# Kernel tuning notes

Measured on AMD Instinct MI355X. Metric: run time of the kernel, lower is better.

The kernel has to match this reference:

```python
import jax, jax.numpy as jnp
import numpy as np

# conv_ada hyperparameters from init_kwargs: ka=1, alpha=0.25, kw=0.2
KA1 = 1.0          # activation scale for conv1 (ka)
KA2 = 1.25         # activation scale for conv2 (ka + alpha)
KW = 0.2           # weight clipping threshold used by the binary weight STE


def ste_sign(x, clip=1.0):
    """Binary sign with straight-through estimator (hardtanh-style clip).
    Forward value is sign(x); gradient is that of clip(x, -clip, clip)."""
    xc = jnp.clip(x, -clip, clip)
    return xc + jax.lax.stop_gradient(jnp.sign(x) - xc)


def conv_bin(x, w, ka, kw):
    """1-bit activation / 1-bit weight 3x3 conv (conv_ada).
    Activations -> ka * sign(x); weights -> per-out-channel mean(|w|) * sign(w)."""
    xq = ka * ste_sign(x)
    alpha_w = jnp.mean(jnp.abs(w), axis=(1, 2, 3), keepdims=True)  # [O,1,1,1]
    wq = alpha_w * ste_sign(w, kw)
    return jax.lax.conv_general_dilated(
        xq, wq, window_strides=(1, 1), padding='SAME',
        dimension_numbers=('NCHW', 'OIHW', 'NCHW'))


def prelu(x, slope):
    # per-channel PReLU, slope shape [C]
    return jnp.where(x >= 0, x, slope[None, :, None, None] * x)


def pixel_shuffle(x, r=2):
    b, c, h, w = x.shape
    co = c // (r * r)
    x = x.reshape(b, co, r, r, h, w)
    x = x.transpose(0, 1, 4, 2, 5, 3)  # b, co, h, r, w, r
    return x.reshape(b, co, h * r, w * r)


def setup_inputs() -> dict:
    key = jax.random.key(0)
    ks = jax.random.split(key, 11)
    B, C, H, W = 8, 64, 256, 256
    return {
        'x': jax.random.normal(ks[0], (B, C, H, W), jnp.float32),
        'w1': jax.random.normal(ks[1], (C, C, 3, 3), jnp.float32) * 0.1,
        'w2': jax.random.normal(ks[2], (2 * C, C, 3, 3), jnp.float32) * 0.1,
        'b_in': jax.random.normal(ks[3], (1, C, 1, 1), jnp.float32) * 0.01,
        'b1': jax.random.normal(ks[4], (1, C, 1, 1), jnp.float32) * 0.01,
        's1': jax.random.uniform(ks[5], (C,), jnp.float32) * 0.25,
        'b2': jax.random.normal(ks[6], (1, C, 1, 1), jnp.float32) * 0.01,
        'b2_': jax.random.normal(ks[7], (1, C, 1, 1), jnp.float32) * 0.01,
        'b3': jax.random.normal(ks[8], (1, 2 * C, 1, 1), jnp.float32) * 0.01,
        's2': jax.random.uniform(ks[9], (2 * C,), jnp.float32) * 0.25,
        'b4': jax.random.normal(ks[10], (1, 2 * C, 1, 1), jnp.float32) * 0.01,
    }


def reference(x, w1, w2, b_in, b1, s1, b2, b2_, b3, s2, b4):
    out = conv_bin(x + b_in, w1, KA1, KW)       # move1_ -> conv1
    xres = out + x                              # residual x = out + x
    # NOTE: in the original forward, move1 -> prelu1 -> move2 are computed on
    # `out` and then immediately overwritten by out = move2_(x); that branch
    # is dead code and does not affect the output (b1, s1, b2 get zero grads).
    out = conv_bin(xres + b2_, w2, KA2, KW)     # move2_ -> conv2
    out = out + jnp.concatenate([xres, xres], axis=1)  # shortcut = cat(x, x)
    out = prelu(out + b3, s2) + b4              # move3 -> prelu2 -> move4
    return pixel_shuffle(out, 2)                # [B, C/2, 2H, 2W]
```

## Files before the change

kernel.cpp:

```cpp
#include <hip/hip_runtime.h>
#include <hip/hip_bf16.h>

typedef unsigned long long u64;
typedef unsigned short ushort8 __attribute__((ext_vector_type(8)));

#define IMG_H 256
#define IMG_W 256
#define CIN   64
#define HW    (IMG_H * IMG_W)
#define NPIX  (8 * HW)

static __device__ __forceinline__ float bf16bits_to_f32(unsigned short h) {
    union { unsigned int u; float f; } c;
    c.u = ((unsigned int)h) << 16;
    return c.f;
}

__global__ void prep_kernel(const float* __restrict__ w1,
                            const float* __restrict__ w2,
                            u64* __restrict__ w1b, float* __restrict__ a1,
                            u64* __restrict__ w2b, float* __restrict__ a2) {
    int blk = blockIdx.x;
    int lane = threadIdx.x;
    const float* w;
    u64* wb;
    float* al;
    if (blk < 64) { w = w1 + (size_t)blk * 576;        wb = w1b + blk * 9;        al = a1 + blk; }
    else          { w = w2 + (size_t)(blk - 64) * 576; wb = w2b + (blk - 64) * 9; al = a2 + (blk - 64); }

    const float* wi = w + lane * 9;
    float s = 0.f;
    u64 bits[9];
#pragma unroll
    for (int t = 0; t < 9; ++t) {
        float v = wi[t];
        s += fabsf(v);
        bits[t] = __ballot(v > 0.f);
    }
#pragma unroll
    for (int m = 32; m >= 1; m >>= 1) s += __shfl_xor(s, m);
    if (lane == 0) {
        *al = s * (1.f / 576.f);
#pragma unroll
        for (int t = 0; t < 9; ++t) wb[t] = bits[t];
    }
}

__global__ __launch_bounds__(256)
void pack_kernel(const float* __restrict__ x,
                 const float* __restrict__ b_in,
                 u64* __restrict__ bits1) {
    int i = blockIdx.x * 256 + threadIdx.x;
    int n = i >> 16, p = i & 65535;
    const float* xp = x + (size_t)n * CIN * HW + p;
    u64 w = 0;
#pragma unroll
    for (int c = 0; c < 64; ++c)
        w |= (u64)((xp[(size_t)c * HW] + b_in[c]) > 0.f) << c;
    bits1[i] = w;
}

__global__ __launch_bounds__(256)
void conv1_kernel(const float* __restrict__ x,
                  const float* __restrict__ b2_,
                  const u64* __restrict__ bits1,
                  const u64* __restrict__ wbits,
                  const float* __restrict__ alpha1,
                  ushort8* __restrict__ xres,
                  u64* __restrict__ bits2) {
    int i = blockIdx.x * 256 + threadIdx.x;
    int n = i >> 16, p = i & 65535;
    int y = p >> 8, xc = p & 255;

    u64 xb[9];
    int invmask = 0, nv = 0;
#pragma unroll
    for (int t = 0; t < 9; ++t) {
        int dy = t / 3 - 1, dx = t % 3 - 1;
        bool v = ((unsigned)(y + dy) < (unsigned)IMG_H) &
                 ((unsigned)(xc + dx) < (unsigned)IMG_W);
        xb[t] = v ? bits1[i + dy * IMG_W + dx] : 0ull;
        invmask |= (v ? 0 : 1) << t;
        nv += v ? 1 : 0;
    }

    const float* xp = x + (size_t)n * CIN * HW + p;
    u64 w2 = 0;

#pragma unroll 1
    for (int g = 0; g < 8; ++g) {
        ushort8 pk;
#pragma unroll
        for (int j = 0; j < 8; ++j) {
            int o = g * 8 + j;
            const u64* wo = wbits + o * 9;
            int D = 0;
#pragma unroll
            for (int t = 0; t < 9; ++t) D += __popcll(xb[t] ^ wo[t]);
            int S = 64 * nv - 2 * D;
            if (invmask) {
                int Dc = 0;
#pragma unroll
                for (int t = 0; t < 9; ++t)
                    if ((invmask >> t) & 1) Dc += __popcll(wo[t]);
                S += 2 * Dc;
            }
            float r = alpha1[o] * (float)S + xp[(size_t)o * HW];
            __hip_bfloat16 hb = __float2bfloat16(r);
            pk[j] = *(unsigned short*)&hb;
            w2 |= (u64)((r + b2_[o]) > 0.f) << o;
        }
        xres[(size_t)(n * 8 + g) * HW + p] = pk;
    }
    bits2[i] = w2;
}

__global__ __launch_bounds__(256)
void conv2_kernel(const ushort8* __restrict__ xres,
                  const u64* __restrict__ bits2,
                  const u64* __restrict__ wbits,
                  const float* __restrict__ alpha2,
                  const float* __restrict__ b3,
                  const float* __restrict__ s2,
                  const float* __restrict__ b4,
                  float* __restrict__ out) {
    int i = blockIdx.x * 256 + threadIdx.x;
    int n = i >> 16, p = i & 65535;
    int y = p >> 8, xc = p & 255;

    u64 xb[9];
    int invmask = 0, nv = 0;
#pragma unroll
    for (int t = 0; t < 9; ++t) {
        int dy = t / 3 - 1, dx = t % 3 - 1;
        bool v = ((unsigned)(y + dy) < (unsigned)IMG_H) &
                 ((unsigned)(xc + dx) < (unsigned)IMG_W);
        xb[t] = v ? bits2[i + dy * IMG_W + dx] : 0ull;
        invmask |= (v ? 0 : 1) << t;
        nv += v ? 1 : 0;
    }

    float* ob = out + (size_t)n * 32 * 512 * 512;
    const int Y = 2 * y, X = 2 * xc;

#pragma unroll 1
    for (int g = 0; g < 8; ++g) {
        ushort8 xr = xres[(size_t)(n * 8 + g) * HW + p];
        float vlo[8], vhi[8];
#pragma unroll
        for (int j = 0; j < 8; ++j) {
            int o = g * 8 + j;
            float xrv = bf16bits_to_f32(xr[j]);
            {
                const u64* wo = wbits + o * 9;
                int D = 0;
#pragma unroll
                for (int t = 0; t < 9; ++t) D += __popcll(xb[t] ^ wo[t]);
                int S = 64 * nv - 2 * D;
                if (invmask) {
                    int Dc = 0;
#pragma unroll
                    for (int t = 0; t < 9; ++t)
                        if ((invmask >> t) & 1) Dc += __popcll(wo[t]);
                    S += 2 * Dc;
                }
                float u = 1.25f * alpha2[o] * (float)S + xrv + b3[o];
                u = (u >= 0.f) ? u : s2[o] * u;
                vlo[j] = u + b4[o];
            }
            {
                int o2 = o + 64;
                const u64* wo = wbits + o2 * 9;
                int D = 0;
#pragma unroll
                for (int t = 0; t < 9; ++t) D += __popcll(xb[t] ^ wo[t]);
                int S = 64 * nv - 2 * D;
                if (invmask) {
                    int Dc = 0;
#pragma unroll
                    for (int t = 0; t < 9; ++t)
                        if ((invmask >> t) & 1) Dc += __popcll(wo[t]);
                    S += 2 * Dc;
                }
                float u = 1.25f * alpha2[o2] * (float)S + xrv + b3[o2];
                u = (u >= 0.f) ? u : s2[o2] * u;
                vhi[j] = u + b4[o2];
            }
        }
#pragma unroll
        for (int jj = 0; jj < 8; jj += 2) {
            int o = g * 8 + jj;
            int co = o >> 2;
            int r1 = (o >> 1) & 1;
            *(float2*)(ob + ((size_t)co * 512 + Y + r1) * 512 + X) =
                make_float2(vlo[jj], vlo[jj + 1]);
            *(float2*)(ob + ((size_t)(co + 16) * 512 + Y + r1) * 512 + X) =
                make_float2(vhi[jj], vhi[jj + 1]);
        }
    }
}

extern "C" void kernel_launch(void* const* d_in, const int* in_sizes, int n_in,
                              void* d_out, int out_size, void* d_ws, size_t ws_size,
                              hipStream_t stream) {
    const float* x    = (const float*)d_in[0];
    const float* w1   = (const float*)d_in[1];
    const float* w2   = (const float*)d_in[2];
    const float* b_in = (const float*)d_in[3];
    const float* b2_  = (const float*)d_in[7];
    const float* b3   = (const float*)d_in[8];
    const float* s2   = (const float*)d_in[9];
    const float* b4   = (const float*)d_in[10];
    float* out = (float*)d_out;

    char* ws = (char*)d_ws;
    u64*   w1b   = (u64*)(ws + 0);
    u64*   w2b   = (u64*)(ws + 4608);
    float* a1    = (float*)(ws + 13824);
    float* a2    = (float*)(ws + 14080);
    u64*   bits1 = (u64*)(ws + 16384);
    u64*   bits2 = (u64*)(ws + 16384 + 4194304);
    ushort8* xres = (ushort8*)(ws + 16384 + 2 * 4194304);

    prep_kernel<<<192, 64, 0, stream>>>(w1, w2, w1b, a1, w2b, a2);

    const int nblk = NPIX / 256;
    pack_kernel <<<nblk, 256, 0, stream>>>(x, b_in, bits1);
    conv1_kernel<<<nblk, 256, 0, stream>>>(x, b2_, bits1, w1b, a1, xres, bits2);
    conv2_kernel<<<nblk, 256, 0, stream>>>(xres, bits2, w2b, a2, b3, s2, b4, out);
}
```

Before: 241.6 us.

## Process two adjacent pixels per thread in pack and binary conv kernels

Each thread in the pack, conv1 and conv2 kernels now handles two horizontally adjacent pixels. The two 3x3 windows share one 3x4 window of bit words (12 loads instead of 18), and each weight word is reused for both pixels. Input reads and output writes become wider vectors (float2 loads, u64x2 and 16-element bf16 stores, float4 output stores), and the grid is halved to match. In exchange each thread uses more registers. The 32-byte residual elements are indexed by the even pixel index, so the residual buffer uses twice the workspace footprint as before.

```diff
diff --git a/kernel.cpp b/kernel.cpp
--- a/kernel.cpp
+++ b/kernel.cpp
@@ -2,7 +2,8 @@
 #include <hip/hip_bf16.h>
 
 typedef unsigned long long u64;
-typedef unsigned short ushort8 __attribute__((ext_vector_type(8)));
+typedef unsigned short ushortx16 __attribute__((ext_vector_type(16)));
+typedef u64 u64x2 __attribute__((ext_vector_type(2)));
 
 #define IMG_H 256
 #define IMG_W 256
@@ -14,6 +15,10 @@
     union { unsigned int u; float f; } c;
     c.u = ((unsigned int)h) << 16;
     return c.f;
+}
+static __device__ __forceinline__ unsigned short f32_to_bf16bits(float f) {
+    __hip_bfloat16 hb = __float2bfloat16(f);
+    return *(unsigned short*)&hb;
 }
 
 __global__ void prep_kernel(const float* __restrict__ w1,
@@ -50,15 +55,22 @@
 void pack_kernel(const float* __restrict__ x,
                  const float* __restrict__ b_in,
                  u64* __restrict__ bits1) {
-    int i = blockIdx.x * 256 + threadIdx.x;
-    int n = i >> 16, p = i & 65535;
+    int tid = blockIdx.x * 256 + threadIdx.x;
+    int n = tid >> 15;
+    int p = (tid & 32767) * 2;
     const float* xp = x + (size_t)n * CIN * HW + p;
-    u64 w = 0;
-#pragma unroll
-    for (int c = 0; c < 64; ++c)
-        w |= (u64)((xp[(size_t)c * HW] + b_in[c]) > 0.f) << c;
-    bits1[i] = w;
-}
+    u64 w0 = 0, w1 = 0;
+#pragma unroll 16
+    for (int c = 0; c < 64; ++c) {
+        float2 v = *(const float2*)(xp + (size_t)c * HW);
+        float b = b_in[c];
+        w0 |= (u64)((v.x + b) > 0.f) << c;
+        w1 |= (u64)((v.y + b) > 0.f) << c;
+    }
+    u64x2 pk; pk.x = w0; pk.y = w1;
+    *(u64x2*)(bits1 + (size_t)n * HW + p) = pk;
+}
+
 
 __global__ __launch_bounds__(256)
 void conv1_kernel(const float* __restrict__ x,
@@ -66,57 +78,88 @@
                   const u64* __restrict__ bits1,
                   const u64* __restrict__ wbits,
                   const float* __restrict__ alpha1,
-                  ushort8* __restrict__ xres,
+                  ushortx16* __restrict__ xres,
                   u64* __restrict__ bits2) {
-    int i = blockIdx.x * 256 + threadIdx.x;
-    int n = i >> 16, p = i & 65535;
+    int tid = blockIdx.x * 256 + threadIdx.x;
+    int n = tid >> 15;
+    int p = (tid & 32767) * 2;
     int y = p >> 8, xc = p & 255;
 
-    u64 xb[9];
-    int invmask = 0, nv = 0;
+    u64 W[3][4];
+    const u64* bp = bits1 + (size_t)n * HW;
+#pragma unroll
+    for (int r = 0; r < 3; ++r) {
+        int yy = y - 1 + r;
+        bool rv = (unsigned)yy < (unsigned)IMG_H;
+        const u64* row = bp + yy * IMG_W + xc;
+        W[r][0] = (rv && xc > 0)   ? row[-1] : 0ull;
+        W[r][1] = rv ? row[0] : 0ull;
+        W[r][2] = rv ? row[1] : 0ull;
+        W[r][3] = (rv && xc < 254) ? row[2]  : 0ull;
+    }
+    int inv0 = 0, inv1 = 0, nv0 = 0, nv1 = 0;
 #pragma unroll
     for (int t = 0; t < 9; ++t) {
-        int dy = t / 3 - 1, dx = t % 3 - 1;
-        bool v = ((unsigned)(y + dy) < (unsigned)IMG_H) &
-                 ((unsigned)(xc + dx) < (unsigned)IMG_W);
-        xb[t] = v ? bits1[i + dy * IMG_W + dx] : 0ull;
-        invmask |= (v ? 0 : 1) << t;
-        nv += v ? 1 : 0;
-    }
+        const int r = t / 3, c = t % 3;
+        bool rv = (unsigned)(y - 1 + r) < (unsigned)IMG_H;
+        bool v0 = rv && !(c == 0 && xc == 0);
+        bool v1 = rv && !(c == 2 && xc == 254);
+        inv0 |= (v0 ? 0 : 1) << t; nv0 += v0 ? 1 : 0;
+        inv1 |= (v1 ? 0 : 1) << t; nv1 += v1 ? 1 : 0;
+    }
+    const int edge = inv0 | inv1;
 
     const float* xp = x + (size_t)n * CIN * HW + p;
-    u64 w2 = 0;
+    u64 w2_0 = 0, w2_1 = 0;
+    ushortx16* rp = xres + ((size_t)n * 8) * HW + p;
 
 #pragma unroll 1
     for (int g = 0; g < 8; ++g) {
-        ushort8 pk;
+        float2 rv[8];
+#pragma unroll
+        for (int j = 0; j < 8; ++j)
+            rv[j] = *(const float2*)(xp + (size_t)(g * 8 + j) * HW);
+
+        ushortx16 pk;
 #pragma unroll
         for (int j = 0; j < 8; ++j) {
             int o = g * 8 + j;
             const u64* wo = wbits + o * 9;
-            int D = 0;
-#pragma unroll
-            for (int t = 0; t < 9; ++t) D += __popcll(xb[t] ^ wo[t]);
-            int S = 64 * nv - 2 * D;
-            if (invmask) {
-                int Dc = 0;
-#pragma unroll
-                for (int t = 0; t < 9; ++t)
-                    if ((invmask >> t) & 1) Dc += __popcll(wo[t]);
-                S += 2 * Dc;
+            int D0 = 0, D1 = 0;
+#pragma unroll
+            for (int t = 0; t < 9; ++t) {
+                const int r = t / 3, c = t % 3;
+                u64 w = wo[t];
+                D0 += __popcll(W[r][c] ^ w);
+                D1 += __popcll(W[r][c + 1] ^ w);
             }
-            float r = alpha1[o] * (float)S + xp[(size_t)o * HW];
-            __hip_bfloat16 hb = __float2bfloat16(r);
-            pk[j] = *(unsigned short*)&hb;
-            w2 |= (u64)((r + b2_[o]) > 0.f) << o;
+            int S0 = 64 * nv0 - 2 * D0;
+            int S1 = 64 * nv1 - 2 * D1;
+            if (edge) {
+#pragma unroll
+                for (int t = 0; t < 9; ++t) {
+                    int pw = __popcll(wo[t]);
+                    if ((inv0 >> t) & 1) S0 += 2 * pw;
+                    if ((inv1 >> t) & 1) S1 += 2 * pw;
+                }
+            }
+            float a = alpha1[o];
+            float r0 = a * (float)S0 + rv[j].x;
+            float r1 = a * (float)S1 + rv[j].y;
+            pk[j]     = f32_to_bf16bits(r0);
+            pk[8 + j] = f32_to_bf16bits(r1);
+            float b2v = b2_[o];
+            w2_0 |= (u64)((r0 + b2v) > 0.f) << o;
+            w2_1 |= (u64)((r1 + b2v) > 0.f) << o;
         }
-        xres[(size_t)(n * 8 + g) * HW + p] = pk;
-    }
-    bits2[i] = w2;
+        rp[(size_t)g * HW] = pk;
+    }
+    u64x2 bw; bw.x = w2_0; bw.y = w2_1;
+    *(u64x2*)(bits2 + (size_t)n * HW + p) = bw;
 }
 
 __global__ __launch_bounds__(256)
-void conv2_kernel(const ushort8* __restrict__ xres,
+void conv2_kernel(const ushortx16* __restrict__ xres,
                   const u64* __restrict__ bits2,
                   const u64* __restrict__ wbits,
                   const float* __restrict__ alpha2,
@@ -124,78 +167,116 @@
                   const float* __restrict__ s2,
                   const float* __restrict__ b4,
                   float* __restrict__ out) {
-    int i = blockIdx.x * 256 + threadIdx.x;
-    int n = i >> 16, p = i & 65535;
+    int tid = blockIdx.x * 256 + threadIdx.x;
+    int n = tid >> 15;
+    int p = (tid & 32767) * 2;
     int y = p >> 8, xc = p & 255;
 
-    u64 xb[9];
-    int invmask = 0, nv = 0;
+    u64 W[3][4];
+    const u64* bp = bits2 + (size_t)n * HW;
+#pragma unroll
+    for (int r = 0; r < 3; ++r) {
+        int yy = y - 1 + r;
+        bool rv = (unsigned)yy < (unsigned)IMG_H;
+        const u64* row = bp + yy * IMG_W + xc;
+        W[r][0] = (rv && xc > 0)   ? row[-1] : 0ull;
+        W[r][1] = rv ? row[0] : 0ull;
+        W[r][2] = rv ? row[1] : 0ull;
+        W[r][3] = (rv && xc < 254) ? row[2]  : 0ull;
+    }
+    int inv0 = 0, inv1 = 0, nv0 = 0, nv1 = 0;
 #pragma unroll
     for (int t = 0; t < 9; ++t) {
-        int dy = t / 3 - 1, dx = t % 3 - 1;
-        bool v = ((unsigned)(y + dy) < (unsigned)IMG_H) &
-                 ((unsigned)(xc + dx) < (unsigned)IMG_W);
-        xb[t] = v ? bits2[i + dy * IMG_W + dx] : 0ull;
-        invmask |= (v ? 0 : 1) << t;
-        nv += v ? 1 : 0;
-    }
-
+        const int r = t / 3, c = t % 3;
+        bool rv = (unsigned)(y - 1 + r) < (unsigned)IMG_H;
+        bool v0 = rv && !(c == 0 && xc == 0);
+        bool v1 = rv && !(c == 2 && xc == 254);
+        inv0 |= (v0 ? 0 : 1) << t; nv0 += v0 ? 1 : 0;
+        inv1 |= (v1 ? 0 : 1) << t; nv1 += v1 ? 1 : 0;
+    }
+    const int edge = inv0 | inv1;
+
+    const ushortx16* xrp = xres + ((size_t)n * 8) * HW + p;
     float* ob = out + (size_t)n * 32 * 512 * 512;
     const int Y = 2 * y, X = 2 * xc;
 
 #pragma unroll 1
     for (int g = 0; g < 8; ++g) {
-        ushort8 xr = xres[(size_t)(n * 8 + g) * HW + p];
-        float vlo[8], vhi[8];
-#pragma unroll
-        for (int j = 0; j < 8; ++j) {
-            int o = g * 8 + j;
-            float xrv = bf16bits_to_f32(xr[j]);
-            {
-                const u64* wo = wbits + o * 9;
-                int D = 0;
-#pragma unroll
-                for (int t = 0; t < 9; ++t) D += __popcll(xb[t] ^ wo[t]);
-                int S = 64 * nv - 2 * D;
-                if (invmask) {
-                    int Dc = 0;
-#pragma unroll
-                    for (int t = 0; t < 9; ++t)
-                        if ((invmask >> t) & 1) Dc += __popcll(wo[t]);
-                    S += 2 * Dc;
+        ushortx16 xr = xrp[(size_t)g * HW];
+
+#pragma unroll
+        for (int jj = 0; jj < 8; jj += 2) {
+            float lo[4], hi[4];
+#pragma unroll
+            for (int q = 0; q < 2; ++q) {
+                int o = g * 8 + jj + q;
+                float xrv0 = bf16bits_to_f32(xr[jj + q]);
+                float xrv1 = bf16bits_to_f32(xr[8 + jj + q]);
+                {
+                    const u64* wo = wbits + o * 9;
+                    int D0 = 0, D1 = 0;
+#pragma unroll
+                    for (int t = 0; t < 9; ++t) {
+                        const int r = t / 3, c = t % 3;
+                        u64 w = wo[t];
+                        D0 += __popcll(W[r][c] ^ w);
+                        D1 += __popcll(W[r][c + 1] ^ w);
+                    }
+                    int S0 = 64 * nv0 - 2 * D0;
+                    int S1 = 64 * nv1 - 2 * D1;
+                    if (edge) {
+#pragma unroll
+                        for (int t = 0; t < 9; ++t) {
+                            int pw = __popcll(wo[t]);
+                            if ((inv0 >> t) & 1) S0 += 2 * pw;
+                            if ((inv1 >> t) & 1) S1 += 2 * pw;
+                        }
+                    }
+                    float ka = 1.25f * alpha2[o], bb = b3[o], ss = s2[o], b4v = b4[o];
+                    float u0 = ka * (float)S0 + xrv0 + bb;
+                    float u1 = ka * (float)S1 + xrv1 + bb;
+                    u0 = (u0 >= 0.f) ? u0 : ss * u0;
+                    u1 = (u1 >= 0.f) ? u1 : ss * u1;
+                    lo[q] = u0 + b4v;
+                    lo[2 + q] = u1 + b4v;
                 }
-                float u = 1.25f * alpha2[o] * (float)S + xrv + b3[o];
-                u = (u >= 0.f) ? u : s2[o] * u;
-                vlo[j] = u + b4[o];
+                {
+                    int o2 = o + 64;
+                    const u64* wo = wbits + o2 * 9;
+                    int D0 = 0, D1 = 0;
+#pragma unroll
+                    for (int t = 0; t < 9; ++t) {
+                        const int r = t / 3, c = t % 3;
+                        u64 w = wo[t];
+                        D0 += __popcll(W[r][c] ^ w);
+                        D1 += __popcll(W[r][c + 1] ^ w);
+                    }
+                    int S0 = 64 * nv0 - 2 * D0;
+                    int S1 = 64 * nv1 - 2 * D1;
+                    if (edge) {
+#pragma unroll
+                        for (int t = 0; t < 9; ++t) {
+                            int pw = __popcll(wo[t]);
+                            if ((inv0 >> t) & 1) S0 += 2 * pw;
+                            if ((inv1 >> t) & 1) S1 += 2 * pw;
+                        }
+                    }
+                    float ka = 1.25f * alpha2[o2], bb = b3[o2], ss = s2[o2], b4v = b4[o2];
+                    float u0 = ka * (float)S0 + xrv0 + bb;
+                    float u1 = ka * (float)S1 + xrv1 + bb;
+                    u0 = (u0 >= 0.f) ? u0 : ss * u0;
+                    u1 = (u1 >= 0.f) ? u1 : ss * u1;
+                    hi[q] = u0 + b4v;
+                    hi[2 + q] = u1 + b4v;
+                }
             }
-            {
-                int o2 = o + 64;
-                const u64* wo = wbits + o2 * 9;
-                int D = 0;
-#pragma unroll
-                for (int t = 0; t < 9; ++t) D += __popcll(xb[t] ^ wo[t]);
-                int S = 64 * nv - 2 * D;
-                if (invmask) {
-                    int Dc = 0;
-#pragma unroll
-                    for (int t = 0; t < 9; ++t)
-                        if ((invmask >> t) & 1) Dc += __popcll(wo[t]);
-                    S += 2 * Dc;
-                }
-                float u = 1.25f * alpha2[o2] * (float)S + xrv + b3[o2];
-                u = (u >= 0.f) ? u : s2[o2] * u;
-                vhi[j] = u + b4[o2];
-            }
-        }
-#pragma unroll
-        for (int jj = 0; jj < 8; jj += 2) {
             int o = g * 8 + jj;
             int co = o >> 2;
             int r1 = (o >> 1) & 1;
-            *(float2*)(ob + ((size_t)co * 512 + Y + r1) * 512 + X) =
-                make_float2(vlo[jj], vlo[jj + 1]);
-            *(float2*)(ob + ((size_t)(co + 16) * 512 + Y + r1) * 512 + X) =
-                make_float2(vhi[jj], vhi[jj + 1]);
+            *(float4*)(ob + ((size_t)co * 512 + Y + r1) * 512 + X) =
+                make_float4(lo[0], lo[1], lo[2], lo[3]);
+            *(float4*)(ob + ((size_t)(co + 16) * 512 + Y + r1) * 512 + X) =
+                make_float4(hi[0], hi[1], hi[2], hi[3]);
         }
     }
 }
@@ -220,11 +301,11 @@
     float* a2    = (float*)(ws + 14080);
     u64*   bits1 = (u64*)(ws + 16384);
     u64*   bits2 = (u64*)(ws + 16384 + 4194304);
-    ushort8* xres = (ushort8*)(ws + 16384 + 2 * 4194304);
+    ushortx16* xres = (ushortx16*)(ws + 16384 + 2 * 4194304);
 
     prep_kernel<<<192, 64, 0, stream>>>(w1, w2, w1b, a1, w2b, a2);
 
-    const int nblk = NPIX / 256;
+    const int nblk = NPIX / 512;
     pack_kernel <<<nblk, 256, 0, stream>>>(x, b_in, bits1);
     conv1_kernel<<<nblk, 256, 0, stream>>>(x, b2_, bits1, w1b, a1, xres, bits2);
     conv2_kernel<<<nblk, 256, 0, stream>>>(xres, bits2, w2b, a2, b3, s2, b4, out);
```

After: 259.8 us. 1.08x slower.
